# Performance work log

Hardware: AMD Instinct MI355X
Metric: run time of the kernel (lower is better)

The kernel has to match this reference:

```python
import jax, jax.numpy as jnp
import numpy as np

B, S, D_IN, D_OUT = 8, 2048, 1024, 1024


def setup_inputs() -> dict:
    key = jax.random.key(0)
    ks = jax.random.split(key, 9)
    sc = 1.0 / np.sqrt(D_IN)
    return {
        "in_k": jax.random.normal(ks[0], (B, S, D_IN), jnp.float32),
        "in_q": jax.random.normal(ks[1], (B, S, D_IN), jnp.float32),
        "in_v": jax.random.normal(ks[2], (B, S, D_IN), jnp.float32),
        "Wk": jax.random.normal(ks[3], (D_IN, D_OUT), jnp.float32) * sc,
        "bk": jax.random.normal(ks[4], (D_OUT,), jnp.float32) * sc,
        "Wq": jax.random.normal(ks[5], (D_IN, D_OUT), jnp.float32) * sc,
        "bq": jax.random.normal(ks[6], (D_OUT,), jnp.float32) * sc,
        "Wv": jax.random.normal(ks[7], (D_IN, D_OUT), jnp.float32) * sc,
        "bv": jax.random.normal(ks[8], (D_OUT,), jnp.float32) * sc,
    }


def reference(in_k, in_q, in_v, Wk, bk, Wq, bq, Wv, bv):
    k = in_k @ Wk + bk  # [B,S,D]
    q = in_q @ Wq + bq
    v = in_v @ Wv + bv
    scale = 1.0 / jnp.sqrt(jnp.asarray(D_OUT, q.dtype))
    scores = jnp.einsum("bqd,bkd->bqk", q, k) * scale  # [B,S,S]
    attn = jax.nn.softmax(scores, axis=-1)
    return jnp.einsum("bqk,bkd->bqd", attn, v)
```

## Files before the change

kernel.cpp:

```cpp
#include <hip/hip_runtime.h>
#include <hip/hip_bf16.h>
#include <stdint.h>

typedef __bf16 bf16x8 __attribute__((ext_vector_type(8)));
typedef float  f32x4  __attribute__((ext_vector_type(4)));
typedef uint16_t u16x8 __attribute__((ext_vector_type(8)));

__device__ __forceinline__ uint16_t f32_to_bf16(float f) {
    union { float f; uint32_t u; } v; v.f = f;
    uint32_t u = v.u;
    uint32_t r = (u + 0x7FFFu + ((u >> 16) & 1u)) >> 16;
    return (uint16_t)r;
}
__device__ __forceinline__ float bf16_to_f32(uint16_t b) {
    union { uint32_t u; float f; } v; v.u = ((uint32_t)b) << 16;
    return v.f;
}

__device__ __forceinline__ void gld16(const uint16_t* g, uint16_t* l) {
    __builtin_amdgcn_global_load_lds(
        (const __attribute__((address_space(1))) void*)g,
        (__attribute__((address_space(3))) void*)l,
        16, 0, 0);
}

__global__ __launch_bounds__(256) void cast_f32_bf16_kernel(
    const float* __restrict__ in, uint16_t* __restrict__ out) {
    size_t i = ((size_t)blockIdx.x * 256 + threadIdx.x) * 4;
    float4 f = *(const float4*)(in + i);
    ushort4 o;
    o.x = f32_to_bf16(f.x); o.y = f32_to_bf16(f.y);
    o.z = f32_to_bf16(f.z); o.w = f32_to_bf16(f.w);
    *(ushort4*)(out + i) = o;
}

__global__ __launch_bounds__(256) void wtrans_kernel(
    const float* __restrict__ W, uint16_t* __restrict__ Wt) {
    __shared__ float tile[64][65];
    const int n0 = blockIdx.x * 64, k0 = blockIdx.y * 64;
    const int tx = threadIdx.x & 63, ty0 = threadIdx.x >> 6;
#pragma unroll
    for (int r = 0; r < 16; ++r) {
        int ty = ty0 + r * 4;
        tile[ty][tx] = W[(size_t)(k0 + ty) * 1024 + n0 + tx];
    }
    __syncthreads();
#pragma unroll
    for (int r = 0; r < 16; ++r) {
        int ty = ty0 + r * 4;
        Wt[(size_t)(n0 + ty) * 1024 + k0 + tx] = f32_to_bf16(tile[tx][ty]);
    }
}

__global__ __launch_bounds__(256) void vtrans_kernel(
    const uint16_t* __restrict__ V, uint16_t* __restrict__ Vt) {
    const int b = blockIdx.z;
    const uint16_t* Vp = V + (size_t)b * 2048 * 1024;
    uint16_t* Vtp = Vt + (size_t)b * 1024 * 2048;
    __shared__ uint16_t tile[64][65];
    const int d0 = blockIdx.x * 64, s0 = blockIdx.y * 64;
    const int tx = threadIdx.x & 63, ty0 = threadIdx.x >> 6;
#pragma unroll
    for (int r = 0; r < 16; ++r) {
        int ty = ty0 + r * 4;
        tile[ty][tx] = Vp[(size_t)(s0 + ty) * 1024 + d0 + tx];
    }
    __syncthreads();
#pragma unroll
    for (int r = 0; r < 16; ++r) {
        int ty = ty0 + r * 4;
        Vtp[(size_t)(d0 + ty) * 2048 + s0 + tx] = tile[tx][ty];
    }
}

template <bool OUT_BF16, bool HAS_BIAS>
__global__ __launch_bounds__(256, 2) void gemm_nt_kernel(
    const uint16_t* __restrict__ A, long long lda, long long sAz,
    const uint16_t* __restrict__ B, long long ldb, long long sBz,
    void* __restrict__ Cv, long long ldc, long long sCz,
    int K, float alpha, const float* __restrict__ bias) {
    __shared__ __align__(16) uint16_t As[128 * 32];
    __shared__ __align__(16) uint16_t Bs[128 * 32];

    const int tid  = threadIdx.x;
    const int lane = tid & 63;
    const int wave = tid >> 6;
    const int z = blockIdx.z;
    A += (size_t)z * sAz;
    B += (size_t)z * sBz;
    const int row0 = blockIdx.y * 128;
    const int col0 = blockIdx.x * 128;

    const int c0 = tid, c1 = tid + 256;
    const int ar0 = c0 >> 2, ak0 = (c0 & 3) * 8;
    const int ar1 = c1 >> 2, ak1 = (c1 & 3) * 8;

    const int wr = wave >> 1, wc = wave & 1;
    const int mrow = lane & 15;
    const int quad = lane >> 4;

    f32x4 acc[4][4];
#pragma unroll
    for (int i = 0; i < 4; ++i)
#pragma unroll
        for (int j = 0; j < 4; ++j) acc[i][j] = 0.0f;

    for (int k0 = 0; k0 < K; k0 += 32) {
        __syncthreads();
        gld16(A + (size_t)(row0 + ar0) * lda + k0 + ak0, &As[(size_t)c0 * 8]);
        gld16(A + (size_t)(row0 + ar1) * lda + k0 + ak1, &As[(size_t)c1 * 8]);
        gld16(B + (size_t)(col0 + ar0) * ldb + k0 + ak0, &Bs[(size_t)c0 * 8]);
        gld16(B + (size_t)(col0 + ar1) * ldb + k0 + ak1, &Bs[(size_t)c1 * 8]);
        __syncthreads();

        bf16x8 af[4], bfj[4];
#pragma unroll
        for (int i = 0; i < 4; ++i)
            af[i] = *(const bf16x8*)&As[(size_t)(wr * 64 + i * 16 + mrow) * 32 + quad * 8];
#pragma unroll
        for (int j = 0; j < 4; ++j)
            bfj[j] = *(const bf16x8*)&Bs[(size_t)(wc * 64 + j * 16 + mrow) * 32 + quad * 8];
#pragma unroll
        for (int i = 0; i < 4; ++i)
#pragma unroll
            for (int j = 0; j < 4; ++j)
                acc[i][j] = __builtin_amdgcn_mfma_f32_16x16x32_bf16(
                    af[i], bfj[j], acc[i][j], 0, 0, 0);
    }

    if (OUT_BF16) {
        uint16_t* C = (uint16_t*)Cv + (size_t)z * sCz;
#pragma unroll
        for (int i = 0; i < 4; ++i)
#pragma unroll
            for (int j = 0; j < 4; ++j)
#pragma unroll
                for (int r = 0; r < 4; ++r) {
                    int row = row0 + wr * 64 + i * 16 + quad * 4 + r;
                    int col = col0 + wc * 64 + j * 16 + mrow;
                    float val = acc[i][j][r] * alpha;
                    if (HAS_BIAS) val += bias[col];
                    C[(size_t)row * ldc + col] = f32_to_bf16(val);
                }
    } else {
        float* C = (float*)Cv + (size_t)z * sCz;
#pragma unroll
        for (int i = 0; i < 4; ++i)
#pragma unroll
            for (int j = 0; j < 4; ++j)
#pragma unroll
                for (int r = 0; r < 4; ++r) {
                    int row = row0 + wr * 64 + i * 16 + quad * 4 + r;
                    int col = col0 + wc * 64 + j * 16 + mrow;
                    float val = acc[i][j][r] * alpha;
                    if (HAS_BIAS) val += bias[col];
                    C[(size_t)row * ldc + col] = val;
                }
    }
}

__global__ __launch_bounds__(256) void softmax_kernel(uint16_t* __restrict__ Sc) {
    __shared__ float red[4];
    uint16_t* p = Sc + (size_t)blockIdx.x * 2048;
    const int tid = threadIdx.x;
    u16x8 v = *(const u16x8*)(p + tid * 8);
    float f[8];
#pragma unroll
    for (int i = 0; i < 8; ++i) f[i] = bf16_to_f32(v[i]);

    float m = f[0];
#pragma unroll
    for (int i = 1; i < 8; ++i) m = fmaxf(m, f[i]);
#pragma unroll
    for (int off = 32; off; off >>= 1) m = fmaxf(m, __shfl_xor(m, off, 64));
    if ((tid & 63) == 0) red[tid >> 6] = m;
    __syncthreads();
    m = fmaxf(fmaxf(red[0], red[1]), fmaxf(red[2], red[3]));

    float e[8], s = 0.0f;
#pragma unroll
    for (int i = 0; i < 8; ++i) { e[i] = __expf(f[i] - m); s += e[i]; }
#pragma unroll
    for (int off = 32; off; off >>= 1) s += __shfl_xor(s, off, 64);
    __syncthreads();
    if ((tid & 63) == 0) red[tid >> 6] = s;
    __syncthreads();
    s = (red[0] + red[1]) + (red[2] + red[3]);
    float inv = 1.0f / s;

    u16x8 o;
#pragma unroll
    for (int i = 0; i < 8; ++i) o[i] = f32_to_bf16(e[i] * inv);
    *(u16x8*)(p + tid * 8) = o;
}

extern "C" void kernel_launch(void* const* d_in, const int* in_sizes, int n_in,
                              void* d_out, int out_size, void* d_ws, size_t ws_size,
                              hipStream_t stream) {
    const float* in_k = (const float*)d_in[0];
    const float* in_q = (const float*)d_in[1];
    const float* in_v = (const float*)d_in[2];
    const float* Wk = (const float*)d_in[3];
    const float* bk = (const float*)d_in[4];
    const float* Wq = (const float*)d_in[5];
    const float* bq = (const float*)d_in[6];
    const float* Wv = (const float*)d_in[7];
    const float* bv = (const float*)d_in[8];
    float* out = (float*)d_out;

    char* w = (char*)d_ws;
    uint16_t* Xq  = (uint16_t*)(w + 0);
    uint16_t* Xk  = (uint16_t*)(w + 33554432);
    uint16_t* Xv  = (uint16_t*)(w + 67108864);
    uint16_t* Qb  = (uint16_t*)(w + 100663296);
    uint16_t* Kb  = (uint16_t*)(w + 134217728);
    uint16_t* Vb  = (uint16_t*)(w + 167772160);
    uint16_t* Wqt = (uint16_t*)(w + 201326592);
    uint16_t* Wkt = (uint16_t*)(w + 203423744);
    uint16_t* Wvt = (uint16_t*)(w + 205520896);
    uint16_t* Sc  = Xq;
    uint16_t* Vt  = Xv;

    cast_f32_bf16_kernel<<<16384, 256, 0, stream>>>(in_q, Xq);
    cast_f32_bf16_kernel<<<16384, 256, 0, stream>>>(in_k, Xk);
    cast_f32_bf16_kernel<<<16384, 256, 0, stream>>>(in_v, Xv);
    wtrans_kernel<<<dim3(16, 16), 256, 0, stream>>>(Wq, Wqt);
    wtrans_kernel<<<dim3(16, 16), 256, 0, stream>>>(Wk, Wkt);
    wtrans_kernel<<<dim3(16, 16), 256, 0, stream>>>(Wv, Wvt);

    gemm_nt_kernel<true, true><<<dim3(8, 128, 1), 256, 0, stream>>>(
        Xq, 1024, 0, Wqt, 1024, 0, Qb, 1024, 0, 1024, 1.0f, bq);
    gemm_nt_kernel<true, true><<<dim3(8, 128, 1), 256, 0, stream>>>(
        Xk, 1024, 0, Wkt, 1024, 0, Kb, 1024, 0, 1024, 1.0f, bk);
    gemm_nt_kernel<true, true><<<dim3(8, 128, 1), 256, 0, stream>>>(
        Xv, 1024, 0, Wvt, 1024, 0, Vb, 1024, 0, 1024, 1.0f, bv);

    vtrans_kernel<<<dim3(16, 32, 8), 256, 0, stream>>>(Vb, Vt);

    gemm_nt_kernel<true, false><<<dim3(16, 16, 8), 256, 0, stream>>>(
        Qb, 1024, 2048LL * 1024, Kb, 1024, 2048LL * 1024,
        Sc, 2048, 2048LL * 2048, 1024, 0.03125f, nullptr);

    softmax_kernel<<<16384, 256, 0, stream>>>(Sc);

    gemm_nt_kernel<false, false><<<dim3(8, 16, 8), 256, 0, stream>>>(
        Sc, 2048, 2048LL * 2048, Vt, 2048, 1024LL * 2048,
        out, 1024, 2048LL * 1024, 2048, 1.0f, nullptr);
}
```

Before: 607.8 us.

## Swizzle GEMM LDS layout and remap blocks into grouped bands for L2 reuse

```diff
diff --git a/kernel.cpp b/kernel.cpp
--- a/kernel.cpp
+++ b/kernel.cpp
@@ -78,26 +78,38 @@
     const uint16_t* __restrict__ A, long long lda, long long sAz,
     const uint16_t* __restrict__ B, long long ldb, long long sBz,
     void* __restrict__ Cv, long long ldc, long long sCz,
-    int K, float alpha, const float* __restrict__ bias) {
+    int K, float alpha, const float* __restrict__ bias,
+    int Z, int tN) {
     __shared__ __align__(16) uint16_t As[128 * 32];
     __shared__ __align__(16) uint16_t Bs[128 * 32];
 
     const int tid  = threadIdx.x;
     const int lane = tid & 63;
     const int wave = tid >> 6;
-    const int z = blockIdx.z;
+
+    const int bid = blockIdx.x;
+    const int z = bid % Z;
+    const int t = bid / Z;
+    const int bandSz = tN * 8;
+    const int band = t / bandSz;
+    const int r0 = t - band * bandSz;
+    const int my = band * 8 + (r0 & 7);
+    const int mx = r0 >> 3;
+
     A += (size_t)z * sAz;
     B += (size_t)z * sBz;
-    const int row0 = blockIdx.y * 128;
-    const int col0 = blockIdx.x * 128;
+    const int row0 = my * 128;
+    const int col0 = mx * 128;
 
     const int c0 = tid, c1 = tid + 256;
-    const int ar0 = c0 >> 2, ak0 = (c0 & 3) * 8;
-    const int ar1 = c1 >> 2, ak1 = (c1 & 3) * 8;
+    const int ar0 = c0 >> 2, ak0 = (((c0 & 3) ^ ((ar0 >> 1) & 3))) * 8;
+    const int ar1 = c1 >> 2, ak1 = (((c1 & 3) ^ ((ar1 >> 1) & 3))) * 8;
 
     const int wr = wave >> 1, wc = wave & 1;
     const int mrow = lane & 15;
     const int quad = lane >> 4;
+    const int sw = (mrow >> 1) & 3;
+    const int qsw = (quad ^ sw) * 8;
 
     f32x4 acc[4][4];
 #pragma unroll
@@ -116,10 +128,10 @@
         bf16x8 af[4], bfj[4];
 #pragma unroll
         for (int i = 0; i < 4; ++i)
-            af[i] = *(const bf16x8*)&As[(size_t)(wr * 64 + i * 16 + mrow) * 32 + quad * 8];
+            af[i] = *(const bf16x8*)&As[(size_t)(wr * 64 + i * 16 + mrow) * 32 + qsw];
 #pragma unroll
         for (int j = 0; j < 4; ++j)
-            bfj[j] = *(const bf16x8*)&Bs[(size_t)(wc * 64 + j * 16 + mrow) * 32 + quad * 8];
+            bfj[j] = *(const bf16x8*)&Bs[(size_t)(wc * 64 + j * 16 + mrow) * 32 + qsw];
 #pragma unroll
         for (int i = 0; i < 4; ++i)
 #pragma unroll
@@ -228,22 +240,22 @@
     wtrans_kernel<<<dim3(16, 16), 256, 0, stream>>>(Wk, Wkt);
     wtrans_kernel<<<dim3(16, 16), 256, 0, stream>>>(Wv, Wvt);
 
-    gemm_nt_kernel<true, true><<<dim3(8, 128, 1), 256, 0, stream>>>(
-        Xq, 1024, 0, Wqt, 1024, 0, Qb, 1024, 0, 1024, 1.0f, bq);
-    gemm_nt_kernel<true, true><<<dim3(8, 128, 1), 256, 0, stream>>>(
-        Xk, 1024, 0, Wkt, 1024, 0, Kb, 1024, 0, 1024, 1.0f, bk);
-    gemm_nt_kernel<true, true><<<dim3(8, 128, 1), 256, 0, stream>>>(
-        Xv, 1024, 0, Wvt, 1024, 0, Vb, 1024, 0, 1024, 1.0f, bv);
+    gemm_nt_kernel<true, true><<<1024, 256, 0, stream>>>(
+        Xq, 1024, 0, Wqt, 1024, 0, Qb, 1024, 0, 1024, 1.0f, bq, 1, 8);
+    gemm_nt_kernel<true, true><<<1024, 256, 0, stream>>>(
+        Xk, 1024, 0, Wkt, 1024, 0, Kb, 1024, 0, 1024, 1.0f, bk, 1, 8);
+    gemm_nt_kernel<true, true><<<1024, 256, 0, stream>>>(
+        Xv, 1024, 0, Wvt, 1024, 0, Vb, 1024, 0, 1024, 1.0f, bv, 1, 8);
 
     vtrans_kernel<<<dim3(16, 32, 8), 256, 0, stream>>>(Vb, Vt);
 
-    gemm_nt_kernel<true, false><<<dim3(16, 16, 8), 256, 0, stream>>>(
+    gemm_nt_kernel<true, false><<<2048, 256, 0, stream>>>(
         Qb, 1024, 2048LL * 1024, Kb, 1024, 2048LL * 1024,
-        Sc, 2048, 2048LL * 2048, 1024, 0.03125f, nullptr);
+        Sc, 2048, 2048LL * 2048, 1024, 0.03125f, nullptr, 8, 16);
 
     softmax_kernel<<<16384, 256, 0, stream>>>(Sc);
 
-    gemm_nt_kernel<false, false><<<dim3(8, 16, 8), 256, 0, stream>>>(
+    gemm_nt_kernel<false, false><<<1024, 256, 0, stream>>>(
         Sc, 2048, 2048LL * 2048, Vt, 2048, 1024LL * 2048,
-        out, 1024, 2048LL * 1024, 2048, 1.0f, nullptr);
-}
+        out, 1024, 2048LL * 1024, 2048, 1.0f, nullptr, 8, 8);
+}
```

Measured after the change: 553.3 us. 1.1x faster.
